# Kernel optimization log

Hardware: AMD Instinct MI355X
Metric: run time of the kernel (lower is better)

The kernel has to match this reference:

```python
import jax, jax.numpy as jnp
import numpy as np

M = 4  # num_modals
EPS = 1e-6


def setup_inputs() -> dict:
    key = jax.random.key(0)
    ks = jax.random.split(key, 12)
    c, h, r, B, n = 768, 3072, 16, 4, 1024
    inp = {
        "x": jax.random.normal(ks[0], (M * B, n, c), jnp.float32),
        "fc1_w": jax.random.normal(ks[1], (h, c), jnp.float32) * 0.02,
        "fc1_b": jax.random.normal(ks[2], (h,), jnp.float32) * 0.02,
        "fc2_w": jax.random.normal(ks[3], (c, h), jnp.float32) * 0.02,
        "fc2_b": jax.random.normal(ks[4], (c,), jnp.float32) * 0.02,
        "a_fc1": jax.random.normal(ks[5], (M, r, c), jnp.float32) * 0.02,
        "b_fc1": jax.random.normal(ks[6], (M, h, r), jnp.float32) * 0.02,
        "a_fc2": jax.random.normal(ks[7], (M, r, h), jnp.float32) * 0.02,
        "b_fc2": jax.random.normal(ks[8], (M, c, r), jnp.float32) * 0.02,
        "gate_w": jax.random.normal(ks[9], (M, M, c), jnp.float32) * 0.02,
        "gate_b": jax.random.normal(ks[10], (M, M), jnp.float32) * 0.02,
        "modality_mask": jax.random.randint(ks[11], (M, B), 0, 2, jnp.int32),
    }
    return inp


def _fused_combine(rw, mask_f, lora):
    # rw: [M,B,n,M] routing softmax; mask_f: [M,B]; lora: [M,B,n,d]
    # per_routing_weights[i,j,t,k] = rw[i,j,t,k] * mask[k,j], renormalized over k
    masked = rw * mask_f.T[None, :, None, :]                      # [M,B,n,M]
    norm = masked / (jnp.sum(masked, axis=-1, keepdims=True) + EPS)
    fused = jnp.einsum("ibnk,kbnd->ibnd", norm, lora)             # combine experts
    return fused * mask_f[:, :, None, None]                       # rows with mask==0 stay zero


def reference(x, fc1_w, fc1_b, fc2_w, fc2_b, a_fc1, b_fc1, a_fc2, b_fc2,
              gate_w, gate_b, modality_mask):
    bs_m, n, c = x.shape
    B = bs_m // M
    xm = x.reshape(M, B, n, c)
    mask_f = modality_mask.astype(x.dtype)                        # [M,B]

    # base fc1
    x1 = (jnp.einsum("ibnc,hc->ibnh", xm, fc1_w) + fc1_b)         # [M,B,n,h]

    # per-modality routing softmax over M experts (computed in fp32 as in torch)
    logits = jnp.einsum("ibnc,iec->ibne", xm, gate_w) + gate_b[:, None, None, :]
    rw = jax.nn.softmax(logits.astype(jnp.float32), axis=-1).astype(x.dtype)

    # HiRA delta for fc1: elementwise(fc1_w, B@A) per modality
    delta1 = fc1_w[None] * jnp.einsum("ihr,irc->ihc", b_fc1, a_fc1)  # [M,h,c]
    lora1 = jnp.einsum("ibnc,ihc->ibnh", xm, delta1)              # [M,B,n,h]

    x1 = x1 + _fused_combine(rw, mask_f, lora1)
    x1 = jax.nn.gelu(x1, approximate=False)                       # mlp.act

    # base fc2
    x2 = jnp.einsum("ibnh,ch->ibnc", x1, fc2_w) + fc2_b           # [M,B,n,c]

    # HiRA delta for fc2
    delta2 = fc2_w[None] * jnp.einsum("icr,irh->ich", b_fc2, a_fc2)  # [M,c,h]
    lora2 = jnp.einsum("ibnh,ich->ibnc", x1, delta2)              # [M,B,n,c]

    x2 = x2 + _fused_combine(rw, mask_f, lora2)
    return x2.reshape(bs_m, n, c)
```

## Files before the change

kernel.cpp:

```cpp
#include <hip/hip_runtime.h>
#include <hip/hip_bf16.h>
#include <math.h>

#define NMOD 4
#define NB 4
#define NTOKN 1024
#define CDIM 768
#define HDIM 3072
#define RDIM 16
#define MROWS (NMOD*NB*NTOKN)
#define RPM (NB*NTOKN)

typedef __bf16 bf16_t;
typedef __bf16 bf16x4 __attribute__((ext_vector_type(4)));
typedef __bf16 bf16x8 __attribute__((ext_vector_type(8)));
typedef float f32x4 __attribute__((ext_vector_type(4)));

__global__ void delta1_kernel(const float* __restrict__ fc1w, const float* __restrict__ a1,
                              const float* __restrict__ b1, bf16_t* __restrict__ out,
                              bf16_t* __restrict__ w_bf) {
  int idx = blockIdx.x * blockDim.x + threadIdx.x;
  if (idx >= NMOD*HDIM*(CDIM/4)) return;
  int c4 = (idx % (CDIM/4)) * 4;
  int h  = (idx / (CDIM/4)) % HDIM;
  int k  = idx / ((CDIM/4)*HDIM);
  const float* brow  = b1 + ((size_t)k*HDIM + h)*RDIM;
  const float* abase = a1 + (size_t)k*RDIM*CDIM + c4;
  float4 s = make_float4(0.f, 0.f, 0.f, 0.f);
  #pragma unroll
  for (int r = 0; r < RDIM; ++r) {
    const float br = brow[r];
    const float4 av = *reinterpret_cast<const float4*>(abase + (size_t)r*CDIM);
    s.x += br*av.x; s.y += br*av.y; s.z += br*av.z; s.w += br*av.w;
  }
  const float4 wv = *reinterpret_cast<const float4*>(fc1w + (size_t)h*CDIM + c4);
  bf16x4 o;
  o[0] = (bf16_t)(wv.x*s.x); o[1] = (bf16_t)(wv.y*s.y);
  o[2] = (bf16_t)(wv.z*s.z); o[3] = (bf16_t)(wv.w*s.w);
  *reinterpret_cast<bf16x4*>(out + ((size_t)k*HDIM + h)*CDIM + c4) = o;
  if (k == 0) {
    bf16x4 w4;
    w4[0] = (bf16_t)wv.x; w4[1] = (bf16_t)wv.y; w4[2] = (bf16_t)wv.z; w4[3] = (bf16_t)wv.w;
    *reinterpret_cast<bf16x4*>(w_bf + (size_t)h*CDIM + c4) = w4;
  }
}

__global__ void delta2_kernel(const float* __restrict__ fc2w, const float* __restrict__ a2,
                              const float* __restrict__ b2, bf16_t* __restrict__ out,
                              bf16_t* __restrict__ w_bf) {
  int idx = blockIdx.x * blockDim.x + threadIdx.x;
  if (idx >= NMOD*CDIM*(HDIM/4)) return;
  int h4 = (idx % (HDIM/4)) * 4;
  int c  = (idx / (HDIM/4)) % CDIM;
  int k  = idx / ((HDIM/4)*CDIM);
  const float* brow  = b2 + ((size_t)k*CDIM + c)*RDIM;
  const float* abase = a2 + (size_t)k*RDIM*HDIM + h4;
  float4 s = make_float4(0.f, 0.f, 0.f, 0.f);
  #pragma unroll
  for (int r = 0; r < RDIM; ++r) {
    const float br = brow[r];
    const float4 av = *reinterpret_cast<const float4*>(abase + (size_t)r*HDIM);
    s.x += br*av.x; s.y += br*av.y; s.z += br*av.z; s.w += br*av.w;
  }
  const float4 wv = *reinterpret_cast<const float4*>(fc2w + (size_t)c*HDIM + h4);
  bf16x4 o;
  o[0] = (bf16_t)(wv.x*s.x); o[1] = (bf16_t)(wv.y*s.y);
  o[2] = (bf16_t)(wv.z*s.z); o[3] = (bf16_t)(wv.w*s.w);
  *reinterpret_cast<bf16x4*>(out + ((size_t)k*CDIM + c)*HDIM + h4) = o;
  if (k == 0) {
    bf16x4 w4;
    w4[0] = (bf16_t)wv.x; w4[1] = (bf16_t)wv.y; w4[2] = (bf16_t)wv.z; w4[3] = (bf16_t)wv.w;
    *reinterpret_cast<bf16x4*>(w_bf + (size_t)c*HDIM + h4) = w4;
  }
}

__global__ void gate_kernel(const float* __restrict__ x, const float* __restrict__ gw,
                            const float* __restrict__ gb, const int* __restrict__ mask,
                            float* __restrict__ normw, bf16_t* __restrict__ x_bf) {
  int t = blockIdx.x * 4 + (threadIdx.x >> 6);
  int lane = threadIdx.x & 63;
  int i = t >> 12;
  int b = (t >> 10) & 3;
  const float4* xr4 = reinterpret_cast<const float4*>(x + (size_t)t * CDIM);
  const float4* gw4 = reinterpret_cast<const float4*>(gw);
  bf16x4* xo4 = reinterpret_cast<bf16x4*>(x_bf + (size_t)t * CDIM);
  float acc[NMOD] = {0.f, 0.f, 0.f, 0.f};
  #pragma unroll
  for (int j = 0; j < 3; ++j) {
    const int q = lane + j*64;
    const float4 xv = xr4[q];
    bf16x4 o;
    o[0] = (bf16_t)xv.x; o[1] = (bf16_t)xv.y; o[2] = (bf16_t)xv.z; o[3] = (bf16_t)xv.w;
    xo4[q] = o;
    #pragma unroll
    for (int e = 0; e < NMOD; ++e) {
      const float4 gv = gw4[(size_t)(i*NMOD + e)*(CDIM/4) + q];
      acc[e] += xv.x*gv.x + xv.y*gv.y + xv.z*gv.z + xv.w*gv.w;
    }
  }
  #pragma unroll
  for (int e = 0; e < NMOD; ++e) {
    float v = acc[e];
    #pragma unroll
    for (int off = 32; off > 0; off >>= 1) v += __shfl_xor(v, off);
    acc[e] = v;
  }
  if (lane == 0) {
    float lg[NMOD], mx = -1e30f;
    #pragma unroll
    for (int e = 0; e < NMOD; ++e) { lg[e] = acc[e] + gb[i*NMOD + e]; mx = fmaxf(mx, lg[e]); }
    float s = 0.f;
    #pragma unroll
    for (int e = 0; e < NMOD; ++e) { lg[e] = expf(lg[e] - mx); s += lg[e]; }
    float inv = 1.f / s;
    float num[NMOD], den = 0.f;
    #pragma unroll
    for (int k = 0; k < NMOD; ++k) {
      float mk = (float)mask[k*NB + b];
      num[k] = lg[k] * inv * mk;
      den += num[k];
    }
    float mi = (float)mask[i*NB + b];
    float scale = mi / (den + 1e-6f);
    #pragma unroll
    for (int k = 0; k < NMOD; ++k) normw[(size_t)t*4 + k] = num[k] * scale;
  }
}

#define BMT 128
#define BNT 128
#define BKT 64

__device__ __forceinline__ void gload_lds16(const bf16_t* g, bf16_t* l) {
  __builtin_amdgcn_global_load_lds((const __attribute__((address_space(1))) void*)g,
                                   (__attribute__((address_space(3))) void*)l, 16, 0, 0);
}
#define MFMA_BF16 __builtin_amdgcn_mfma_f32_16x16x32_bf16

__global__ __launch_bounds__(256, 4)
void gemm_kernel(const bf16_t* __restrict__ A, const bf16_t* __restrict__ W0,
                 const bf16_t* __restrict__ WL, const float* __restrict__ bias,
                 const int* __restrict__ mask,
                 bf16_t* __restrict__ outB, bf16_t* __restrict__ outL,
                 int K, int N, int P, int modStride, int rowOff, int posOff) {
  __shared__ __align__(16) bf16_t As[BMT * BKT];
  __shared__ __align__(16) bf16_t Bs[BNT * BKT];

  const int tid  = threadIdx.x;
  const int lane = tid & 63;
  const int wv   = tid >> 6;
  const int wr   = wv >> 1, wc = wv & 1;
  const int row0 = blockIdx.x * BMT;
  const int col0 = blockIdx.y * BNT;
  const bool lora = (blockIdx.z != 0);

  const int mod = row0 / P;
  if (lora) {
    const int bb = (posOff + (row0 % P)) >> 10;
    if (mask[mod*NB + bb] == 0) return;
  }
  const int gArow0 = mod * modStride + rowOff + (row0 % P);
  const bf16_t* Wp = lora ? (WL + (size_t)mod * N * K) : W0;

  const int ldr = tid >> 3;
  const int ssl = ((tid & 7) ^ (ldr & 7)) * 8;
  const bf16_t* Ag = A  + (size_t)(gArow0 + ldr) * K + ssl;
  const bf16_t* Wg = Wp + (size_t)(col0   + ldr) * K + ssl;

  const int fr  = lane & 15;
  const int hi  = lane >> 4;
  const int sk0 = ((hi)     ^ (fr & 7)) * 8;
  const int sk1 = ((4 + hi) ^ (fr & 7)) * 8;

  f32x4 acc[4][4];
  #pragma unroll
  for (int i = 0; i < 4; ++i)
    #pragma unroll
    for (int j = 0; j < 4; ++j) acc[i][j] = (f32x4){0.f, 0.f, 0.f, 0.f};

  for (int k0 = 0; k0 < K; k0 += BKT) {
    __syncthreads();
    #pragma unroll
    for (int j = 0; j < 4; ++j)
      gload_lds16(Ag + (size_t)(j*32) * K + k0, &As[tid*8 + j*2048]);
    #pragma unroll
    for (int j = 0; j < 4; ++j)
      gload_lds16(Wg + (size_t)(j*32) * K + k0, &Bs[tid*8 + j*2048]);
    __syncthreads();

    #pragma unroll
    for (int kk = 0; kk < 2; ++kk) {
      const int sk = (kk == 0) ? sk0 : sk1;
      bf16x8 af[4], bfr[4];
      #pragma unroll
      for (int mi = 0; mi < 4; ++mi)
        af[mi] = *reinterpret_cast<const bf16x8*>(&As[(wr*64 + mi*16 + fr)*BKT + sk]);
      #pragma unroll
      for (int ni = 0; ni < 4; ++ni)
        bfr[ni] = *reinterpret_cast<const bf16x8*>(&Bs[(wc*64 + ni*16 + fr)*BKT + sk]);
      #pragma unroll
      for (int mi = 0; mi < 4; ++mi)
        #pragma unroll
        for (int ni = 0; ni < 4; ++ni)
          acc[mi][ni] = MFMA_BF16(af[mi], bfr[ni], acc[mi][ni], 0, 0, 0);
    }
  }

  bf16_t* outp = lora ? outL : outB;
  #pragma unroll
  for (int mi = 0; mi < 4; ++mi) {
    #pragma unroll
    for (int ni = 0; ni < 4; ++ni) {
      const int colg = col0 + wc*64 + ni*16 + fr;
      float bv = 0.f;
      if (!lora) bv = bias[colg];
      #pragma unroll
      for (int rg = 0; rg < 4; ++rg) {
        const int rowg = row0 + wr*64 + mi*16 + hi*4 + rg;
        outp[(size_t)rowg * N + colg] = (bf16_t)(acc[mi][ni][rg] + bv);
      }
    }
  }
}

__global__ void combine1_kernel(bf16_t* __restrict__ base1, const bf16_t* __restrict__ L1,
                                const float* __restrict__ normw, const int* __restrict__ mask,
                                int P, int chunkOff) {
  int idx = blockIdx.x * blockDim.x + threadIdx.x;
  if (idx >= P * (HDIM/8)) return;
  int h0 = (idx % (HDIM/8)) * 8;
  int p  = idx / (HDIM/8);
  const int b = (chunkOff + p) >> 10;
  float lv[4][8];
  #pragma unroll
  for (int k = 0; k < 4; ++k) {
    if (mask[k*NB + b] != 0) {
      f32x4 raw = __builtin_nontemporal_load(
          reinterpret_cast<const f32x4*>(&L1[((size_t)(k*P + p))*HDIM + h0]));
      bf16x8 v = *reinterpret_cast<bf16x8*>(&raw);
      #pragma unroll
      for (int j = 0; j < 8; ++j) lv[k][j] = (float)v[j];
    } else {
      #pragma unroll
      for (int j = 0; j < 8; ++j) lv[k][j] = 0.f;
    }
  }
  #pragma unroll
  for (int i = 0; i < 4; ++i) {
    size_t ro = ((size_t)(i*P + p))*HDIM + h0;
    const float* nw = normw + ((size_t)(i*RPM + chunkOff + p))*4;
    float n0 = nw[0], n1 = nw[1], n2 = nw[2], n3 = nw[3];
    bf16x8 bv = *reinterpret_cast<const bf16x8*>(&base1[ro]);
    bf16x8 ov;
    #pragma unroll
    for (int j = 0; j < 8; ++j) {
      float v = (float)bv[j] + n0*lv[0][j] + n1*lv[1][j] + n2*lv[2][j] + n3*lv[3][j];
      float g = 0.5f * v * (1.f + erff(v * 0.70710678118654752f));
      ov[j] = (bf16_t)g;
    }
    *reinterpret_cast<bf16x8*>(&base1[ro]) = ov;
  }
}

__global__ void combine2_kernel(const bf16_t* __restrict__ base2, const bf16_t* __restrict__ L2,
                                const float* __restrict__ normw, const int* __restrict__ mask,
                                float* __restrict__ out, int P, int chunkOff) {
  int idx = blockIdx.x * blockDim.x + threadIdx.x;
  if (idx >= P * (CDIM/8)) return;
  int c0 = (idx % (CDIM/8)) * 8;
  int p  = idx / (CDIM/8);
  const int b = (chunkOff + p) >> 10;
  float lv[4][8];
  #pragma unroll
  for (int k = 0; k < 4; ++k) {
    if (mask[k*NB + b] != 0) {
      f32x4 raw = __builtin_nontemporal_load(
          reinterpret_cast<const f32x4*>(&L2[((size_t)(k*P + p))*CDIM + c0]));
      bf16x8 v = *reinterpret_cast<bf16x8*>(&raw);
      #pragma unroll
      for (int j = 0; j < 8; ++j) lv[k][j] = (float)v[j];
    } else {
      #pragma unroll
      for (int j = 0; j < 8; ++j) lv[k][j] = 0.f;
    }
  }
  #pragma unroll
  for (int i = 0; i < 4; ++i) {
    int grow = i*RPM + chunkOff + p;
    const float* nw = normw + (size_t)grow*4;
    float n0 = nw[0], n1 = nw[1], n2 = nw[2], n3 = nw[3];
    f32x4 raw = __builtin_nontemporal_load(
        reinterpret_cast<const f32x4*>(&base2[((size_t)(i*P + p))*CDIM + c0]));
    bf16x8 bv = *reinterpret_cast<bf16x8*>(&raw);
    float o[8];
    #pragma unroll
    for (int j = 0; j < 8; ++j)
      o[j] = (float)bv[j] + n0*lv[0][j] + n1*lv[1][j] + n2*lv[2][j] + n3*lv[3][j];
    f32x4* op = reinterpret_cast<f32x4*>(out + (size_t)grow*CDIM + c0);
    __builtin_nontemporal_store((f32x4){o[0], o[1], o[2], o[3]}, op);
    __builtin_nontemporal_store((f32x4){o[4], o[5], o[6], o[7]}, op + 1);
  }
}

extern "C" void kernel_launch(void* const* d_in, const int* in_sizes, int n_in,
                              void* d_out, int out_size, void* d_ws, size_t ws_size,
                              hipStream_t stream) {
  (void)in_sizes; (void)n_in; (void)out_size;
  const float* x    = (const float*)d_in[0];
  const float* fc1w = (const float*)d_in[1];
  const float* fc1b = (const float*)d_in[2];
  const float* fc2w = (const float*)d_in[3];
  const float* fc2b = (const float*)d_in[4];
  const float* a1   = (const float*)d_in[5];
  const float* b1   = (const float*)d_in[6];
  const float* a2   = (const float*)d_in[7];
  const float* b2   = (const float*)d_in[8];
  const float* gw   = (const float*)d_in[9];
  const float* gb   = (const float*)d_in[10];
  const int*   mask = (const int*)d_in[11];
  float* out = (float*)d_out;

  char* ws = (char*)d_ws;
  size_t off = 0;
  auto carve = [&](size_t bytes) -> char* {
    char* p = ws + off; off += (bytes + 255) & ~(size_t)255; return p;
  };
  bf16_t* x_bf  = (bf16_t*)carve((size_t)MROWS*CDIM*2);
  bf16_t* w1_bf = (bf16_t*)carve((size_t)HDIM*CDIM*2);
  bf16_t* w2_bf = (bf16_t*)carve((size_t)CDIM*HDIM*2);
  bf16_t* d1_bf = (bf16_t*)carve((size_t)NMOD*HDIM*CDIM*2);
  bf16_t* d2_bf = (bf16_t*)carve((size_t)NMOD*CDIM*HDIM*2);
  float*  normw = (float*)carve((size_t)MROWS*4*4);
  const size_t fixedBytes = off;

  int P = RPM;
  while (P > 128 && fixedBytes + (size_t)49152*P + 4096 > ws_size) P >>= 1;
  const int NCH = RPM / P;

  bf16_t* base1 = (bf16_t*)carve((size_t)NMOD*P*HDIM*2);
  bf16_t* Lbuf  = (bf16_t*)carve((size_t)NMOD*P*HDIM*2);
  bf16_t* L1    = Lbuf;
  bf16_t* base2 = Lbuf;
  bf16_t* L2    = Lbuf + (size_t)NMOD*P*CDIM;

  delta1_kernel<<<NMOD*HDIM*(CDIM/4)/256, 256, 0, stream>>>(fc1w, a1, b1, d1_bf, w1_bf);
  delta2_kernel<<<NMOD*CDIM*(HDIM/4)/256, 256, 0, stream>>>(fc2w, a2, b2, d2_bf, w2_bf);
  gate_kernel<<<MROWS/4, 256, 0, stream>>>(x, gw, gb, mask, normw, x_bf);

  for (int g = 0; g < NCH; ++g) {
    const int chunkOff = g * P;
    gemm_kernel<<<dim3(NMOD*P/BMT, HDIM/BNT, 2), 256, 0, stream>>>(
        x_bf, w1_bf, d1_bf, fc1b, mask, base1, L1, CDIM, HDIM, P, RPM, chunkOff, chunkOff);
    combine1_kernel<<<(P*(HDIM/8) + 255)/256, 256, 0, stream>>>(base1, L1, normw, mask, P, chunkOff);
    gemm_kernel<<<dim3(NMOD*P/BMT, CDIM/BNT, 2), 256, 0, stream>>>(
        base1, w2_bf, d2_bf, fc2b, mask, base2, L2, HDIM, CDIM, P, P, 0, chunkOff);
    combine2_kernel<<<(P*(CDIM/8) + 255)/256, 256, 0, stream>>>(base2, L2, normw, mask, out, P, chunkOff);
  }
}
```

Before: 418.6 us.

## Split fc1 GEMM and combine into two hidden-dimension halves to shrink LoRA buffer

The fc1 stage now runs as two passes over halves of the hidden dimension, each writing a half-width LoRA intermediate that combine1 consumes right away. This cuts the LoRA scratch buffer by a quarter of the per-row footprint, so larger chunks P fit in the workspace and fewer chunk iterations are needed, and the smaller intermediate may also stay resident in cache between the GEMM and combine. The cost is twice as many launches for the fc1 stage and smaller per-launch grids.

```diff
diff --git a/kernel.cpp b/kernel.cpp
--- a/kernel.cpp
+++ b/kernel.cpp
@@ -7,6 +7,7 @@
 #define NTOKN 1024
 #define CDIM 768
 #define HDIM 3072
+#define HHALF (HDIM/2)
 #define RDIM 16
 #define MROWS (NMOD*NB*NTOKN)
 #define RPM (NB*NTOKN)
@@ -142,7 +143,8 @@
                  const bf16_t* __restrict__ WL, const float* __restrict__ bias,
                  const int* __restrict__ mask,
                  bf16_t* __restrict__ outB, bf16_t* __restrict__ outL,
-                 int K, int N, int P, int modStride, int rowOff, int posOff) {
+                 int K, int N, int ldB, size_t wStride,
+                 int P, int modStride, int rowOff, int posOff) {
   __shared__ __align__(16) bf16_t As[BMT * BKT];
   __shared__ __align__(16) bf16_t Bs[BNT * BKT];
 
@@ -160,7 +162,7 @@
     if (mask[mod*NB + bb] == 0) return;
   }
   const int gArow0 = mod * modStride + rowOff + (row0 % P);
-  const bf16_t* Wp = lora ? (WL + (size_t)mod * N * K) : W0;
+  const bf16_t* Wp = lora ? (WL + (size_t)mod * wStride) : W0;
 
   const int ldr = tid >> 3;
   const int ssl = ((tid & 7) ^ (ldr & 7)) * 8;
@@ -206,37 +208,35 @@
     }
   }
 
-  bf16_t* outp = lora ? outL : outB;
   #pragma unroll
   for (int mi = 0; mi < 4; ++mi) {
     #pragma unroll
     for (int ni = 0; ni < 4; ++ni) {
       const int colg = col0 + wc*64 + ni*16 + fr;
-      float bv = 0.f;
-      if (!lora) bv = bias[colg];
       #pragma unroll
       for (int rg = 0; rg < 4; ++rg) {
         const int rowg = row0 + wr*64 + mi*16 + hi*4 + rg;
-        outp[(size_t)rowg * N + colg] = (bf16_t)(acc[mi][ni][rg] + bv);
+        if (lora) outL[(size_t)rowg * N + colg] = (bf16_t)(acc[mi][ni][rg]);
+        else      outB[(size_t)rowg * ldB + colg] = (bf16_t)(acc[mi][ni][rg] + bias[colg]);
       }
     }
   }
 }
 
-__global__ void combine1_kernel(bf16_t* __restrict__ base1, const bf16_t* __restrict__ L1,
+__global__ void combine1_kernel(bf16_t* __restrict__ base1, const bf16_t* __restrict__ L1h,
                                 const float* __restrict__ normw, const int* __restrict__ mask,
-                                int P, int chunkOff) {
+                                int P, int chunkOff, int hOff) {
   int idx = blockIdx.x * blockDim.x + threadIdx.x;
-  if (idx >= P * (HDIM/8)) return;
-  int h0 = (idx % (HDIM/8)) * 8;
-  int p  = idx / (HDIM/8);
+  if (idx >= P * (HHALF/8)) return;
+  int h0 = (idx % (HHALF/8)) * 8;
+  int p  = idx / (HHALF/8);
   const int b = (chunkOff + p) >> 10;
   float lv[4][8];
   #pragma unroll
   for (int k = 0; k < 4; ++k) {
     if (mask[k*NB + b] != 0) {
       f32x4 raw = __builtin_nontemporal_load(
-          reinterpret_cast<const f32x4*>(&L1[((size_t)(k*P + p))*HDIM + h0]));
+          reinterpret_cast<const f32x4*>(&L1h[((size_t)(k*P + p))*HHALF + h0]));
       bf16x8 v = *reinterpret_cast<bf16x8*>(&raw);
       #pragma unroll
       for (int j = 0; j < 8; ++j) lv[k][j] = (float)v[j];
@@ -247,7 +247,7 @@
   }
   #pragma unroll
   for (int i = 0; i < 4; ++i) {
-    size_t ro = ((size_t)(i*P + p))*HDIM + h0;
+    size_t ro = ((size_t)(i*P + p))*HDIM + hOff + h0;
     const float* nw = normw + ((size_t)(i*RPM + chunkOff + p))*4;
     float n0 = nw[0], n1 = nw[1], n2 = nw[2], n3 = nw[3];
     bf16x8 bv = *reinterpret_cast<const bf16x8*>(&base1[ro]);
@@ -334,12 +334,12 @@
   const size_t fixedBytes = off;
 
   int P = RPM;
-  while (P > 128 && fixedBytes + (size_t)49152*P + 4096 > ws_size) P >>= 1;
+  while (P > 128 && fixedBytes + (size_t)36864*P + 4096 > ws_size) P >>= 1;
   const int NCH = RPM / P;
 
   bf16_t* base1 = (bf16_t*)carve((size_t)NMOD*P*HDIM*2);
-  bf16_t* Lbuf  = (bf16_t*)carve((size_t)NMOD*P*HDIM*2);
-  bf16_t* L1    = Lbuf;
+  bf16_t* Lbuf  = (bf16_t*)carve((size_t)NMOD*P*HHALF*2);
+  bf16_t* L1h   = Lbuf;
   bf16_t* base2 = Lbuf;
   bf16_t* L2    = Lbuf + (size_t)NMOD*P*CDIM;
 
@@ -349,11 +349,19 @@
 
   for (int g = 0; g < NCH; ++g) {
     const int chunkOff = g * P;
-    gemm_kernel<<<dim3(NMOD*P/BMT, HDIM/BNT, 2), 256, 0, stream>>>(
-        x_bf, w1_bf, d1_bf, fc1b, mask, base1, L1, CDIM, HDIM, P, RPM, chunkOff, chunkOff);
-    combine1_kernel<<<(P*(HDIM/8) + 255)/256, 256, 0, stream>>>(base1, L1, normw, mask, P, chunkOff);
+    for (int hh = 0; hh < 2; ++hh) {
+      const int h0 = hh * HHALF;
+      gemm_kernel<<<dim3(NMOD*P/BMT, HHALF/BNT, 2), 256, 0, stream>>>(
+          x_bf, w1_bf + (size_t)h0*CDIM, d1_bf + (size_t)h0*CDIM, fc1b + h0, mask,
+          base1 + h0, L1h, CDIM, HHALF, HDIM, (size_t)HDIM*CDIM,
+          P, RPM, chunkOff, chunkOff);
+      combine1_kernel<<<(P*(HHALF/8) + 255)/256, 256, 0, stream>>>(
+          base1, L1h, normw, mask, P, chunkOff, h0);
+    }
     gemm_kernel<<<dim3(NMOD*P/BMT, CDIM/BNT, 2), 256, 0, stream>>>(
-        base1, w2_bf, d2_bf, fc2b, mask, base2, L2, HDIM, CDIM, P, P, 0, chunkOff);
-    combine2_kernel<<<(P*(CDIM/8) + 255)/256, 256, 0, stream>>>(base2, L2, normw, mask, out, P, chunkOff);
-  }
-}
+        base1, w2_bf, d2_bf, fc2b, mask, base2, L2, HDIM, CDIM, CDIM, (size_t)CDIM*HDIM,
+        P, P, 0, chunkOff);
+    combine2_kernel<<<(P*(CDIM/8) + 255)/256, 256, 0, stream>>>(
+        base2, L2, normw, mask, out, P, chunkOff);
+  }
+}
```

Result: slower. 439.7 us (+5.1%).
